# Kernel optimization log

Hardware: AMD Instinct MI355X
Metric: run time of the kernel (lower is better)

## Reference

```python
import jax, jax.numpy as jnp
import numpy as np

DIM = 1024
CTX_DIM = 1024
HEADS = 16
DIM_HEAD = 64
INNER = HEADS * DIM_HEAD  # 1024
FF_INNER = 4 * DIM        # 4096
EPS = 1e-5


def layer_norm(x, g, b):
    mu = jnp.mean(x, axis=-1, keepdims=True)
    var = jnp.var(x, axis=-1, keepdims=True)
    return (x - mu) * jax.lax.rsqrt(var + EPS) * g + b


def setup_inputs() -> dict:
    key = jax.random.key(0)
    ks = jax.random.split(key, 9)
    b, n, j = 4, 2048, 1024
    inp = {
        "x": jax.random.normal(ks[0], (b, n, DIM), dtype=jnp.float32),
        "context": jax.random.normal(ks[1], (b, j, CTX_DIM), dtype=jnp.float32),
        "ln_g": jnp.ones((DIM,), jnp.float32),
        "ln_b": jnp.zeros((DIM,), jnp.float32),
        "cln_g": jnp.ones((CTX_DIM,), jnp.float32),
        "cln_b": jnp.zeros((CTX_DIM,), jnp.float32),
        "Wq": jax.random.normal(ks[2], (DIM, INNER), dtype=jnp.float32) * (DIM ** -0.5),
        "Wkv": jax.random.normal(ks[3], (CTX_DIM, 2 * DIM_HEAD), dtype=jnp.float32) * (CTX_DIM ** -0.5),
        "Wo": jax.random.normal(ks[4], (INNER, DIM), dtype=jnp.float32) * (INNER ** -0.5),
        "Wff1": jax.random.normal(ks[5], (DIM, 2 * FF_INNER), dtype=jnp.float32) * (DIM ** -0.5),
        "Wff2": jax.random.normal(ks[6], (FF_INNER, DIM), dtype=jnp.float32) * (FF_INNER ** -0.5),
    }
    return inp


def reference(x, context, ln_g, ln_b, cln_g, cln_b, Wq, Wkv, Wo, Wff1, Wff2):
    scale = DIM_HEAD ** -0.5
    xn = layer_norm(x, ln_g, ln_b)                       # [b, n, dim]
    cn = layer_norm(context, cln_g, cln_b)               # [b, j, ctx_dim]
    b, n, _ = xn.shape
    q = (xn @ Wq).reshape(b, n, HEADS, DIM_HEAD).transpose(0, 2, 1, 3) * scale  # [b,h,n,d]
    kv = cn @ Wkv                                        # [b, j, 2d]
    k, v = kv[..., :DIM_HEAD], kv[..., DIM_HEAD:]        # [b, j, d] each (shared head)
    sim = jnp.einsum('bhid,bjd->bhij', q, k)
    attn = jax.nn.softmax(sim, axis=-1)
    out = jnp.einsum('bhij,bjd->bhid', attn, v)          # [b,h,n,d]
    out = out.transpose(0, 2, 1, 3).reshape(b, n, INNER) @ Wo  # [b,n,dim]
    # parallel SwiGLU FF on normed x
    ff = xn @ Wff1                                       # [b,n,2*ff_inner]
    h, gate = ff[..., :FF_INNER], ff[..., FF_INNER:]
    out = out + (jax.nn.silu(gate) * h) @ Wff2
    return out
```

## Files before the change

kernel.cpp:

```cpp
#include <hip/hip_runtime.h>
#include <math.h>

typedef unsigned short u16;
typedef __attribute__((ext_vector_type(8))) short short8;
typedef __attribute__((ext_vector_type(8))) unsigned short ushortx8;
typedef __attribute__((ext_vector_type(4))) unsigned short ushortx4;
typedef __attribute__((ext_vector_type(4))) float floatx4;

#define DEVI __device__ __forceinline__

DEVI float bf2f(u16 u) {
    unsigned int i = ((unsigned int)u) << 16;
    float f; __builtin_memcpy(&f, &i, 4); return f;
}
DEVI u16 f2bf(float f) {
    unsigned int i; __builtin_memcpy(&i, &f, 4);
    i += 0x7fffu + ((i >> 16) & 1u);
    return (u16)(i >> 16);
}
DEVI void gl_lds16(const void* g, void* l) {
    __builtin_amdgcn_global_load_lds(
        (const __attribute__((address_space(1))) void*)g,
        (__attribute__((address_space(3))) void*)l, 16, 0, 0);
}

template <bool FF1>
__global__ void transpose_kernel(const float* __restrict__ B, u16* __restrict__ BT,
                                 int K, int N) {
    __shared__ u16 t[32][33];
    int nb = blockIdx.x * 32, kb = blockIdx.y * 32;
    int tx = threadIdx.x, ty = threadIdx.y;
    for (int i = ty; i < 32; i += 8)
        t[i][tx] = f2bf(B[(size_t)(kb + i) * N + nb + tx]);
    __syncthreads();
    for (int i = ty; i < 32; i += 8) {
        int c = nb + i;
        int r_out = FF1 ? ((((c & 4095) >> 4) << 5) + ((c >> 12) << 4) + (c & 15)) : c;
        BT[(size_t)r_out * K + kb + tx] = t[tx][i];
    }
}

__global__ __launch_bounds__(256)
void ln_kernel(const float* __restrict__ x, const float* __restrict__ g,
               const float* __restrict__ b, u16* __restrict__ out) {
    __shared__ float sw[4], sw2[4];
    const int tid = threadIdx.x, wave = tid >> 6, lane = tid & 63;
    const float* xr = x + (size_t)blockIdx.x * 1024;
    float4 v = *(const float4*)(xr + tid * 4);
    float f[4] = {v.x, v.y, v.z, v.w};
    float s = f[0] + f[1] + f[2] + f[3];
    float s2 = f[0]*f[0] + f[1]*f[1] + f[2]*f[2] + f[3]*f[3];
    for (int o = 32; o; o >>= 1) {
        s  += __shfl_xor(s,  o, 64);
        s2 += __shfl_xor(s2, o, 64);
    }
    if (lane == 0) { sw[wave] = s; sw2[wave] = s2; }
    __syncthreads();
    float tot  = sw[0] + sw[1] + sw[2] + sw[3];
    float tot2 = sw2[0] + sw2[1] + sw2[2] + sw2[3];
    float mu  = tot * (1.f / 1024.f);
    float var = tot2 * (1.f / 1024.f) - mu * mu;
    float rs  = rsqrtf(var + 1e-5f);
    float4 gv = *(const float4*)(g + tid * 4);
    float4 bv = *(const float4*)(b + tid * 4);
    ushortx4 ov;
    ov[0] = f2bf((f[0] - mu) * rs * gv.x + bv.x);
    ov[1] = f2bf((f[1] - mu) * rs * gv.y + bv.y);
    ov[2] = f2bf((f[2] - mu) * rs * gv.z + bv.z);
    ov[3] = f2bf((f[3] - mu) * rs * gv.w + bv.w);
    *(ushortx4*)(out + (size_t)blockIdx.x * 1024 + tid * 4) = ov;
}

enum { EPI_PLAIN = 0, EPI_Q = 1, EPI_KV = 2, EPI_ADD_F32 = 3 };

template <int EPI>
__global__ __launch_bounds__(256)
void gemm_bt_kernel(const u16* __restrict__ A, const u16* __restrict__ BT,
                    void* __restrict__ Cv, u16* __restrict__ AUX,
                    int M, int N, int K) {
    __shared__ u16 As[128 * 32];
    __shared__ u16 Bs[128 * 32];
    const int tid = threadIdx.x, wave = tid >> 6, lane = tid & 63;
    const int mbase = blockIdx.x * 128, nbase = blockIdx.y * 128;
    const int m0 = (wave & 1) * 64, n0 = (wave >> 1) * 64;
    const int lrow = lane & 15, lq = lane >> 4;

    floatx4 zero = {0.f, 0.f, 0.f, 0.f};
    floatx4 acc[4][4];
#pragma unroll
    for (int i = 0; i < 4; i++)
#pragma unroll
        for (int j = 0; j < 4; j++) acc[i][j] = zero;

    for (int kt = 0; kt < K; kt += 32) {
#pragma unroll
        for (int i = 0; i < 2; i++) {
            int e = i * 2048 + tid * 8;
            int r = e >> 5, c = e & 31;
            gl_lds16(A  + (size_t)(mbase + r) * K + kt + c, As + e);
            gl_lds16(BT + (size_t)(nbase + r) * K + kt + c, Bs + e);
        }
        __syncthreads();
        short8 af[4], bf[4];
#pragma unroll
        for (int f = 0; f < 4; f++) {
            af[f] = *(const short8*)(As + (m0 + f * 16 + lrow) * 32 + lq * 8);
            bf[f] = *(const short8*)(Bs + (n0 + f * 16 + lrow) * 32 + lq * 8);
        }
#pragma unroll
        for (int i = 0; i < 4; i++)
#pragma unroll
            for (int j = 0; j < 4; j++)
                acc[i][j] = __builtin_amdgcn_mfma_f32_16x16x32_bf16(af[i], bf[j], acc[i][j], 0, 0, 0);
        __syncthreads();
    }

#pragma unroll
    for (int mf = 0; mf < 4; mf++)
#pragma unroll
        for (int nf = 0; nf < 4; nf++)
#pragma unroll
            for (int r = 0; r < 4; r++) {
                int row = mbase + m0 + mf * 16 + lq * 4 + r;
                int col = nbase + n0 + nf * 16 + lrow;
                float v = acc[mf][nf][r];
                if constexpr (EPI == EPI_PLAIN) {
                    ((u16*)Cv)[(size_t)row * N + col] = f2bf(v);
                } else if constexpr (EPI == EPI_Q) {
                    int b = row >> 11, i2 = row & 2047, h = col >> 6, d = col & 63;
                    ((u16*)Cv)[((size_t)((b * 16 + h) * 2048 + i2)) * 64 + d] = f2bf(v * 0.125f);
                } else if constexpr (EPI == EPI_KV) {
                    int b = row >> 10, j = row & 1023;
                    if (col < 64) ((u16*)Cv)[(size_t)row * 64 + col] = f2bf(v);
                    else AUX[((size_t)(b * 64 + (col - 64))) * 1024 + j] = f2bf(v);
                } else {
                    ((float*)Cv)[(size_t)row * N + col] = v + bf2f(AUX[(size_t)row * N + col]);
                }
            }
}

__global__ __launch_bounds__(512, 2)
void gemm256_ff1_kernel(const u16* __restrict__ A, const u16* __restrict__ BT,
                        u16* __restrict__ C, int K) {
    extern __shared__ float4 smem4[];
    char* smem = (char*)smem4;

    const int tid = threadIdx.x, wave = tid >> 6, lane = tid & 63;
    const int wm = wave >> 2, wn = wave & 3;
    const int lrow = lane & 15, lq = lane >> 4;

    const int bid = blockIdx.x;
    const int wg = (bid & 7) * 128 + (bid >> 3);
    const int mbase = (wg & 31) * 256, nbase = (wg >> 5) * 256;

    const int sl = (tid & 7) ^ ((tid >> 3) & 7);
    const u16* aBase = A  + (size_t)(mbase + (tid >> 3)) * K + sl * 8;
    const u16* bBase = BT + (size_t)(nbase + (tid >> 3)) * K + sl * 8;
    char* dst0 = smem + tid * 16;

#define STAGE_A(buf_, h_, kt_) do {                                        \
        char* d_ = dst0 + (buf_) * 65536 + (h_) * 16384;                   \
        gl_lds16(aBase + (size_t)(h_) * 128 * K + (kt_), d_);              \
        gl_lds16(aBase + (size_t)((h_) * 128 + 64) * K + (kt_), d_ + 8192);\
    } while (0)
#define STAGE_B(buf_, h_, kt_) do {                                        \
        char* d_ = dst0 + 32768 + (buf_) * 65536 + (h_) * 16384;           \
        gl_lds16(bBase + (size_t)(h_) * 128 * K + (kt_), d_);              \
        gl_lds16(bBase + (size_t)((h_) * 128 + 64) * K + (kt_), d_ + 8192);\
    } while (0)
#define BAR() do { asm volatile("" ::: "memory");                          \
        __builtin_amdgcn_s_barrier();                                      \
        asm volatile("" ::: "memory"); } while (0)
#define LGKM0() do { asm volatile("s_waitcnt lgkmcnt(0)" ::: "memory");    \
        __builtin_amdgcn_sched_barrier(0); } while (0)
#define MFMA16(Q, BF) do {                                                 \
        __builtin_amdgcn_s_setprio(1);                                     \
        _Pragma("unroll") for (int mf_ = 0; mf_ < 4; ++mf_)                \
        _Pragma("unroll") for (int nf_ = 0; nf_ < 2; ++nf_)                \
        _Pragma("unroll") for (int ks_ = 0; ks_ < 2; ++ks_)                \
            acc[Q][mf_][nf_] = __builtin_amdgcn_mfma_f32_16x16x32_bf16(    \
                af[mf_][ks_], BF[nf_][ks_], acc[Q][mf_][nf_], 0, 0, 0);    \
        __builtin_amdgcn_s_setprio(0); } while (0)
#define READ_A(H) do { _Pragma("unroll") for (int mf_ = 0; mf_ < 4; ++mf_){\
        af[mf_][0] = *(const short8*)(Ab + (H) * 16384 + mf_ * 2048 + cb0);\
        af[mf_][1] = *(const short8*)(Ab + (H) * 16384 + mf_ * 2048 + cb1);\
    } } while (0)
#define READ_B(DST, H) do { _Pragma("unroll") for (int nf_ = 0; nf_ < 2; ++nf_){\
        DST[nf_][0] = *(const short8*)(Bb + (H) * 16384 + nf_ * 2048 + cb0);\
        DST[nf_][1] = *(const short8*)(Bb + (H) * 16384 + nf_ * 2048 + cb1);\
    } } while (0)

    floatx4 zero = {0.f, 0.f, 0.f, 0.f};
    floatx4 acc[4][4][2];
#pragma unroll
    for (int q = 0; q < 4; ++q)
#pragma unroll
        for (int i = 0; i < 4; ++i)
#pragma unroll
            for (int j = 0; j < 2; ++j) acc[q][i][j] = zero;

    const int cb0 = ((0 + lq) ^ (lrow & 7)) << 4;
    const int cb1 = ((4 + lq) ^ (lrow & 7)) << 4;

    const int NT = K >> 6;

    STAGE_A(0, 0, 0); STAGE_B(0, 0, 0); STAGE_A(0, 1, 0); STAGE_B(0, 1, 0);
    STAGE_A(1, 0, 64); STAGE_B(1, 0, 64);
    asm volatile("s_waitcnt vmcnt(4)" ::: "memory");
    BAR();

    for (int t = 0; t < NT; ++t) {
        const int bu = t & 1;
        const char* Ab = smem + bu * 65536 + (size_t)((wm * 64 + lrow) * 128);
        const char* Bb = smem + bu * 65536 + 32768 + (size_t)((wn * 32 + lrow) * 128);
        short8 af[4][2], bf0[2][2], bf1[2][2];

        READ_A(0); READ_B(bf0, 0);
        if (t + 1 < NT) STAGE_A(bu ^ 1, 1, (t + 1) * 64);
        BAR(); LGKM0();
        MFMA16(0, bf0);
        BAR();

        READ_B(bf1, 1);
        if (t + 1 < NT) STAGE_B(bu ^ 1, 1, (t + 1) * 64);
        BAR(); LGKM0();
        MFMA16(1, bf1);
        BAR();

        READ_A(1);
        if (t + 2 < NT) STAGE_A(bu, 0, (t + 2) * 64);
        BAR(); LGKM0();
        MFMA16(2, bf0);
        BAR();

        if (t + 2 < NT) STAGE_B(bu, 0, (t + 2) * 64);
        MFMA16(3, bf1);
        asm volatile("s_waitcnt vmcnt(4)" ::: "memory");
        BAR();
    }
#undef STAGE_A
#undef STAGE_B
#undef BAR
#undef LGKM0
#undef MFMA16
#undef READ_A
#undef READ_B

    const int orow = mbase + wm * 64 + lq * 4;
    const int og16 = (nbase >> 5) + wn;
#pragma unroll
    for (int q = 0; q < 4; ++q) {
        const int qm = q >> 1, qn = q & 1;
#pragma unroll
        for (int mf = 0; mf < 4; ++mf)
#pragma unroll
            for (int r = 0; r < 4; ++r) {
                float hv = acc[q][mf][0][r], gv = acc[q][mf][1][r];
                float act = hv * (gv / (1.f + __expf(-gv)));
                int row = orow + qm * 128 + mf * 16 + r;
                int col = (og16 + qn * 4) * 16 + lrow;
                C[(size_t)row * 4096 + col] = f2bf(act);
            }
    }
}

__global__ __launch_bounds__(256)
void attn_kernel(const u16* __restrict__ q, const u16* __restrict__ k,
                 const u16* __restrict__ vt, u16* __restrict__ o) {
    __shared__ char smem[53248];
    u16* Qs  = (u16*)smem;
    u16* Ps  = (u16*)smem;
    u16* Ks  = (u16*)(smem + 17408);
    u16* VTs = (u16*)(smem + 35840);
    float* Lp   = (float*)(smem + 17408);
    float* Ltot = (float*)(smem + 18432);

    const int tid = threadIdx.x, wave = tid >> 6, lane = tid & 63;
    const int lrow = lane & 15, lq = lane >> 4;
    const int b = blockIdx.z, h = blockIdx.y, mt = blockIdx.x;

    const u16* qb = q + ((size_t)((b * 16 + h) * 2048) + mt * 64) * 64;
    const u16* kb = k + (size_t)b * 1024 * 64;
    const u16* vb = vt + (size_t)b * 64 * 1024;

#pragma unroll
    for (int i = 0; i < 2; i++) {
        int e = i * 2048 + tid * 8;
        int r = e >> 6, d = e & 63;
        *(ushortx8*)(Qs + r * 72 + d) = *(const ushortx8*)(qb + e);
    }
    __syncthreads();
    short8 qf[2][4];
#pragma unroll
    for (int ks = 0; ks < 2; ks++)
#pragma unroll
        for (int cf = 0; cf < 4; cf++)
            qf[ks][cf] = *(const short8*)(Qs + (cf * 16 + lrow) * 72 + ks * 32 + lq * 8);

    floatx4 zero = {0.f, 0.f, 0.f, 0.f};
    floatx4 oacc[4];
#pragma unroll
    for (int i = 0; i < 4; i++) oacc[i] = zero;
    float lsum[4] = {0.f, 0.f, 0.f, 0.f};

    for (int jt = 0; jt < 8; jt++) {
#pragma unroll
        for (int i = 0; i < 4; i++) {
            int e = i * 2048 + tid * 8;
            int r = e >> 6, d = e & 63;
            *(ushortx8*)(Ks + r * 72 + d) = *(const ushortx8*)(kb + jt * 8192 + e);
            int dv = e >> 7, jj = e & 127;
            *(ushortx8*)(VTs + dv * 136 + jj) =
                *(const ushortx8*)(vb + (size_t)dv * 1024 + jt * 128 + jj);
        }
        __syncthreads();

        floatx4 sacc[2][4];
#pragma unroll
        for (int rf = 0; rf < 2; rf++)
#pragma unroll
            for (int cf = 0; cf < 4; cf++) sacc[rf][cf] = zero;
#pragma unroll
        for (int ks = 0; ks < 2; ks++) {
            short8 af[2];
#pragma unroll
            for (int rf = 0; rf < 2; rf++)
                af[rf] = *(const short8*)(Ks + (wave * 32 + rf * 16 + lrow) * 72 + ks * 32 + lq * 8);
#pragma unroll
            for (int rf = 0; rf < 2; rf++)
#pragma unroll
                for (int cf = 0; cf < 4; cf++)
                    sacc[rf][cf] = __builtin_amdgcn_mfma_f32_16x16x32_bf16(af[rf], qf[ks][cf], sacc[rf][cf], 0, 0, 0);
        }

#pragma unroll
        for (int rf = 0; rf < 2; rf++)
#pragma unroll
            for (int cf = 0; cf < 4; cf++) {
                float p0 = __expf(sacc[rf][cf][0]);
                float p1 = __expf(sacc[rf][cf][1]);
                float p2 = __expf(sacc[rf][cf][2]);
                float p3 = __expf(sacc[rf][cf][3]);
                lsum[cf] += p0 + p1 + p2 + p3;
                ushortx4 pk = {f2bf(p0), f2bf(p1), f2bf(p2), f2bf(p3)};
                int m = cf * 16 + lrow;
                int j0 = wave * 32 + rf * 16 + lq * 4;
                *(ushortx4*)(Ps + m * 136 + j0) = pk;
            }
        __syncthreads();

#pragma unroll
        for (int ks = 0; ks < 4; ks++) {
            short8 pf[4];
#pragma unroll
            for (int mf = 0; mf < 4; mf++)
                pf[mf] = *(const short8*)(Ps + (mf * 16 + lrow) * 136 + ks * 32 + lq * 8);
            short8 vf = *(const short8*)(VTs + (wave * 16 + lrow) * 136 + ks * 32 + lq * 8);
#pragma unroll
            for (int mf = 0; mf < 4; mf++)
                oacc[mf] = __builtin_amdgcn_mfma_f32_16x16x32_bf16(pf[mf], vf, oacc[mf], 0, 0, 0);
        }
        __syncthreads();
    }

    float lv[4];
#pragma unroll
    for (int cf = 0; cf < 4; cf++) {
        float v = lsum[cf];
        v += __shfl_xor(v, 16, 64);
        v += __shfl_xor(v, 32, 64);
        lv[cf] = v;
    }
    if (lane < 16) {
#pragma unroll
        for (int cf = 0; cf < 4; cf++) Lp[wave * 64 + cf * 16 + lane] = lv[cf];
    }
    __syncthreads();
    if (tid < 64) Ltot[tid] = Lp[tid] + Lp[64 + tid] + Lp[128 + tid] + Lp[192 + tid];
    __syncthreads();

    const int d = wave * 16 + lrow;
    const size_t orow0 = (size_t)(b * 2048 + mt * 64);
#pragma unroll
    for (int mf = 0; mf < 4; mf++)
#pragma unroll
        for (int r = 0; r < 4; r++) {
            int m = mf * 16 + lq * 4 + r;
            float val = oacc[mf][r] / Ltot[m];
            o[(orow0 + m) * 1024 + h * 64 + d] = f2bf(val);
        }
}

extern "C" void kernel_launch(void* const* d_in, const int* in_sizes, int n_in,
                              void* d_out, int out_size, void* d_ws, size_t ws_size,
                              hipStream_t stream) {
    const float* x     = (const float*)d_in[0];
    const float* ctx   = (const float*)d_in[1];
    const float* ln_g  = (const float*)d_in[2];
    const float* ln_b  = (const float*)d_in[3];
    const float* cln_g = (const float*)d_in[4];
    const float* cln_b = (const float*)d_in[5];
    const float* Wq    = (const float*)d_in[6];
    const float* Wkv   = (const float*)d_in[7];
    const float* Wo    = (const float*)d_in[8];
    const float* Wff1  = (const float*)d_in[9];
    const float* Wff2  = (const float*)d_in[10];
    (void)in_sizes; (void)n_in; (void)out_size; (void)ws_size;

    u16* ws = (u16*)d_ws;
    const size_t MiB = 524288;
    u16* ffa   = ws;
    u16* qb    = ws;
    u16* attnb = ws + 16 * MiB;
    u16* cn    = ws + 32 * MiB;
    u16* kb    = ws + 40 * MiB;
    u16* vtb   = ws + 40 * MiB + 262144;
    u16* WqT   = ws + 41 * MiB;
    u16* WkvT  = ws + 43 * MiB;
    u16* WoT   = ws + 44 * MiB;
    u16* xn    = ws + 64 * MiB;
    u16* wo    = ws + 80 * MiB;
    u16* Wff1T = ws + 96 * MiB;
    u16* Wff2T = ws + 112 * MiB;

    static bool attr_set = false;
    if (!attr_set) {
        hipFuncSetAttribute(reinterpret_cast<const void*>(gemm256_ff1_kernel),
                            hipFuncAttributeMaxDynamicSharedMemorySize, 131072);
        attr_set = true;
    }

    dim3 tb(32, 8);
    transpose_kernel<false><<<dim3(32, 32),  tb, 0, stream>>>(Wq,   WqT,   1024, 1024);
    transpose_kernel<false><<<dim3(4, 32),   tb, 0, stream>>>(Wkv,  WkvT,  1024, 128);
    transpose_kernel<false><<<dim3(32, 32),  tb, 0, stream>>>(Wo,   WoT,   1024, 1024);
    transpose_kernel<true> <<<dim3(256, 32), tb, 0, stream>>>(Wff1, Wff1T, 1024, 8192);
    transpose_kernel<false><<<dim3(32, 128), tb, 0, stream>>>(Wff2, Wff2T, 4096, 1024);

    ln_kernel<<<8192, 256, 0, stream>>>(x,   ln_g,  ln_b,  xn);
    ln_kernel<<<4096, 256, 0, stream>>>(ctx, cln_g, cln_b, cn);

    gemm_bt_kernel<EPI_Q> <<<dim3(64, 8), 256, 0, stream>>>(xn, WqT,  qb, nullptr, 8192, 1024, 1024);
    gemm_bt_kernel<EPI_KV><<<dim3(32, 1), 256, 0, stream>>>(cn, WkvT, kb, vtb,     4096, 128,  1024);

    attn_kernel<<<dim3(32, 16, 4), 256, 0, stream>>>(qb, kb, vtb, attnb);

    gemm_bt_kernel<EPI_PLAIN><<<dim3(64, 8), 256, 0, stream>>>(attnb, WoT, wo, nullptr, 8192, 1024, 1024);
    gemm256_ff1_kernel<<<dim3(1024), 512, 131072, stream>>>(xn, Wff1T, ffa, 1024);
    gemm_bt_kernel<EPI_ADD_F32><<<dim3(64, 8), 256, 0, stream>>>(ffa, Wff2T, d_out, wo, 8192, 1024, 4096);
}
```

Measured before the change: 598.9 us.

## Restructure FF1 GEMM pipeline to read full tile once and remap blocks per XCD

```diff
diff --git a/kernel.cpp b/kernel.cpp
--- a/kernel.cpp
+++ b/kernel.cpp
@@ -150,8 +150,9 @@
     const int lrow = lane & 15, lq = lane >> 4;
 
     const int bid = blockIdx.x;
-    const int wg = (bid & 7) * 128 + (bid >> 3);
-    const int mbase = (wg & 31) * 256, nbase = (wg >> 5) * 256;
+    const int xcd = bid & 7, s = bid >> 3;
+    const int mbase = (s >> 2) * 256;
+    const int nbase = (xcd * 4 + (s & 3)) * 256;
 
     const int sl = (tid & 7) ^ ((tid >> 3) & 7);
     const u16* aBase = A  + (size_t)(mbase + (tid >> 3)) * K + sl * 8;
@@ -171,24 +172,14 @@
 #define BAR() do { asm volatile("" ::: "memory");                          \
         __builtin_amdgcn_s_barrier();                                      \
         asm volatile("" ::: "memory"); } while (0)
-#define LGKM0() do { asm volatile("s_waitcnt lgkmcnt(0)" ::: "memory");    \
-        __builtin_amdgcn_sched_barrier(0); } while (0)
-#define MFMA16(Q, BF) do {                                                 \
+#define MFMA16(Q, AF, BF) do {                                             \
         __builtin_amdgcn_s_setprio(1);                                     \
         _Pragma("unroll") for (int mf_ = 0; mf_ < 4; ++mf_)                \
         _Pragma("unroll") for (int nf_ = 0; nf_ < 2; ++nf_)                \
         _Pragma("unroll") for (int ks_ = 0; ks_ < 2; ++ks_)                \
             acc[Q][mf_][nf_] = __builtin_amdgcn_mfma_f32_16x16x32_bf16(    \
-                af[mf_][ks_], BF[nf_][ks_], acc[Q][mf_][nf_], 0, 0, 0);    \
+                AF[mf_][ks_], BF[nf_][ks_], acc[Q][mf_][nf_], 0, 0, 0);    \
         __builtin_amdgcn_s_setprio(0); } while (0)
-#define READ_A(H) do { _Pragma("unroll") for (int mf_ = 0; mf_ < 4; ++mf_){\
-        af[mf_][0] = *(const short8*)(Ab + (H) * 16384 + mf_ * 2048 + cb0);\
-        af[mf_][1] = *(const short8*)(Ab + (H) * 16384 + mf_ * 2048 + cb1);\
-    } } while (0)
-#define READ_B(DST, H) do { _Pragma("unroll") for (int nf_ = 0; nf_ < 2; ++nf_){\
-        DST[nf_][0] = *(const short8*)(Bb + (H) * 16384 + nf_ * 2048 + cb0);\
-        DST[nf_][1] = *(const short8*)(Bb + (H) * 16384 + nf_ * 2048 + cb1);\
-    } } while (0)
 
     floatx4 zero = {0.f, 0.f, 0.f, 0.f};
     floatx4 acc[4][4][2];
@@ -213,38 +204,43 @@
         const int bu = t & 1;
         const char* Ab = smem + bu * 65536 + (size_t)((wm * 64 + lrow) * 128);
         const char* Bb = smem + bu * 65536 + 32768 + (size_t)((wn * 32 + lrow) * 128);
-        short8 af[4][2], bf0[2][2], bf1[2][2];
-
-        READ_A(0); READ_B(bf0, 0);
-        if (t + 1 < NT) STAGE_A(bu ^ 1, 1, (t + 1) * 64);
-        BAR(); LGKM0();
-        MFMA16(0, bf0);
+
+        if (t + 1 < NT) { STAGE_A(bu ^ 1, 1, (t + 1) * 64); STAGE_B(bu ^ 1, 1, (t + 1) * 64); }
+
+        short8 af[4][2], a2[4][2], bf0[2][2], bf1[2][2];
+#pragma unroll
+        for (int mf = 0; mf < 4; ++mf) {
+            af[mf][0] = *(const short8*)(Ab + mf * 2048 + cb0);
+            af[mf][1] = *(const short8*)(Ab + mf * 2048 + cb1);
+        }
+#pragma unroll
+        for (int nf = 0; nf < 2; ++nf) {
+            bf0[nf][0] = *(const short8*)(Bb + nf * 2048 + cb0);
+            bf0[nf][1] = *(const short8*)(Bb + nf * 2048 + cb1);
+            bf1[nf][0] = *(const short8*)(Bb + 16384 + nf * 2048 + cb0);
+            bf1[nf][1] = *(const short8*)(Bb + 16384 + nf * 2048 + cb1);
+        }
+#pragma unroll
+        for (int mf = 0; mf < 4; ++mf) {
+            a2[mf][0] = *(const short8*)(Ab + 16384 + mf * 2048 + cb0);
+            a2[mf][1] = *(const short8*)(Ab + 16384 + mf * 2048 + cb1);
+        }
+
+        MFMA16(0, af, bf0);
+        MFMA16(1, af, bf1);
         BAR();
-
-        READ_B(bf1, 1);
-        if (t + 1 < NT) STAGE_B(bu ^ 1, 1, (t + 1) * 64);
-        BAR(); LGKM0();
-        MFMA16(1, bf1);
-        BAR();
-
-        READ_A(1);
-        if (t + 2 < NT) STAGE_A(bu, 0, (t + 2) * 64);
-        BAR(); LGKM0();
-        MFMA16(2, bf0);
-        BAR();
-
-        if (t + 2 < NT) STAGE_B(bu, 0, (t + 2) * 64);
-        MFMA16(3, bf1);
-        asm volatile("s_waitcnt vmcnt(4)" ::: "memory");
+        if (t + 2 < NT) { STAGE_A(bu, 0, (t + 2) * 64); STAGE_B(bu, 0, (t + 2) * 64); }
+        MFMA16(2, a2, bf0);
+        MFMA16(3, a2, bf1);
+
+        if (t + 2 < NT) asm volatile("s_waitcnt vmcnt(4)" ::: "memory");
+        else            asm volatile("s_waitcnt vmcnt(0)" ::: "memory");
         BAR();
     }
 #undef STAGE_A
 #undef STAGE_B
 #undef BAR
-#undef LGKM0
 #undef MFMA16
-#undef READ_A
-#undef READ_B
 
     const int orow = mbase + wm * 64 + lq * 4;
     const int og16 = (nbase >> 5) + wn;
```

Result: faster. 586.8 us (-2.0%).
